# Kernel optimization log

Measured on AMD Instinct MI355X. Metric: run time of the kernel, lower is better.

Reference implementation:

```python
import jax, jax.numpy as jnp
import numpy as np

N_HEADS = 16
NEG_FILL = -1000000000.0  # masked_fill value from the torch module
PADDING = 0.0             # default padding arg


def setup_inputs() -> dict:
    key = jax.random.key(0)
    kq, kk, kv = jax.random.split(key, 3)
    B, S, D = 2, 2048, 1024
    q = jax.random.normal(kq, (B, S, D), dtype=jnp.float32)
    k = jax.random.normal(kk, (B, S, D), dtype=jnp.float32)
    v = jax.random.normal(kv, (B, S, D), dtype=jnp.float32)
    return {"q": q, "k": k, "v": v, "is_masked": 1}


def reference(q, k, v, is_masked):
    B, S, D = q.shape
    d_key = D // N_HEADS

    def split_heads(x):  # [B,S,D] -> [B,H,S,d_key]
        return x.reshape(B, S, N_HEADS, d_key).transpose(0, 2, 1, 3)

    qh, kh, vh = split_heads(q), split_heads(k), split_heads(v)
    scale = 1.0 / jnp.sqrt(jnp.asarray(d_key, dtype=q.dtype))
    # [B,H,S,S] raw attention scores
    scores = jnp.einsum("bhqd,bhkd->bhqk", qh, kh) * scale
    # value-based mask: keep positions where score != padding
    mask = scores != PADDING
    if is_masked:
        causal = jnp.tril(jnp.ones((S, S), dtype=bool))  # [S,S]
        mask = mask & causal
    scores = jnp.where(mask, scores, jnp.asarray(NEG_FILL, dtype=scores.dtype))
    probs = jax.nn.softmax(scores, axis=-1)
    out = jnp.einsum("bhqk,bhkd->bhqd", probs, vh)  # [B,H,S,d_key]
    return out.transpose(0, 2, 1, 3).reshape(B, S, D)
```

## Files before the change

### kernel.cpp

```cpp
#include <hip/hip_runtime.h>
#include <hip/hip_bf16.h>
#include <math.h>

typedef __bf16   bf16x8 __attribute__((ext_vector_type(8)));
typedef _Float16 f16x4  __attribute__((ext_vector_type(4)));
typedef float    f32x4  __attribute__((ext_vector_type(4)));

#define S_LEN 2048
#define D_MODEL 1024
#define LT 72
#define CEXP 0.18033688011112042f

__device__ __forceinline__ float fast_exp2(float x) {
    return __builtin_amdgcn_exp2f(x);
}

template<bool BF>
__device__ __forceinline__ void body(
    const void* __restrict__ qv, const void* __restrict__ kv,
    const void* __restrict__ vv, void* __restrict__ outv,
    int maskflag, int z, int bh,
    __bf16* Ks0, __bf16* Ks1, _Float16* Vt0, _Float16* Vt1)
{
    const int b    = bh >> 4;
    const int h    = bh & 15;
    const int t    = threadIdx.x;
    const int w    = t >> 6;
    const int lane = t & 63;
    const int m16  = lane & 15;
    const int quad = lane >> 4;

    const int q0 = z * 64;
    const size_t head_off = (size_t)b * S_LEN * D_MODEL + (size_t)h * 64;

    const __bf16* qb = (const __bf16*)qv; const float* qf = (const float*)qv;
    const __bf16* kb = (const __bf16*)kv; const float* kf = (const float*)kv;
    const __bf16* vb = (const __bf16*)vv; const float* vf = (const float*)vv;

    bf16x8 aq0, aq1;
    {
        const int r = q0 + w * 16 + m16;
        if (BF) {
            const __bf16* p = qb + head_off + (size_t)r * D_MODEL;
            aq0 = *(const bf16x8*)&p[quad * 8];
            aq1 = *(const bf16x8*)&p[32 + quad * 8];
            #pragma unroll
            for (int j = 0; j < 8; ++j) {
                aq0[j] = (__bf16)((float)aq0[j] * CEXP);
                aq1[j] = (__bf16)((float)aq1[j] * CEXP);
            }
        } else {
            const float* p = qf + head_off + (size_t)r * D_MODEL;
            #pragma unroll
            for (int half = 0; half < 2; ++half) {
                float4 x0 = *(const float4*)&p[half * 32 + quad * 8];
                float4 x1 = *(const float4*)&p[half * 32 + quad * 8 + 4];
                bf16x8 f = { (__bf16)(x0.x*CEXP), (__bf16)(x0.y*CEXP),
                             (__bf16)(x0.z*CEXP), (__bf16)(x0.w*CEXP),
                             (__bf16)(x1.x*CEXP), (__bf16)(x1.y*CEXP),
                             (__bf16)(x1.z*CEXP), (__bf16)(x1.w*CEXP) };
                if (half == 0) aq0 = f; else aq1 = f;
            }
        }
    }

    f32x4 o[4];
    #pragma unroll
    for (int i = 0; i < 4; ++i) o[i] = (f32x4){0.f,0.f,0.f,0.f};
    float lsum = 0.f;

    const int kg = t >> 4, dg = t & 15;
    const int k0 = kg * 4, d0 = dg * 4;
    const int cst = k0 ^ ((dg & 7) << 3);

    const int ktmax = maskflag ? z : (S_LEN / 64 - 1);

    float4 kr[4], vr[4];
    auto pref = [&](int kt) {
        if (BF) {
            const __bf16* base = kb + head_off + (size_t)kt * 64 * D_MODEL;
            #pragma unroll
            for (int i = 0; i < 2; ++i) {
                int c = t + i * 256, row = c >> 3, off = (c & 7) << 3;
                *(uint4*)&kr[i] = *(const uint4*)&base[(size_t)row * D_MODEL + off];
            }
            const __bf16* vp = vb + head_off + (size_t)(kt * 64 + k0) * D_MODEL + d0;
            #pragma unroll
            for (int j = 0; j < 4; ++j)
                *(uint2*)&vr[j] = *(const uint2*)&vp[(size_t)j * D_MODEL];
        } else {
            const float* base = kf + head_off + (size_t)kt * 64 * D_MODEL;
            #pragma unroll
            for (int i = 0; i < 4; ++i) {
                int c = t + i * 256, row = c >> 4, off = (c & 15) << 2;
                kr[i] = *(const float4*)&base[(size_t)row * D_MODEL + off];
            }
            const float* vp = vf + head_off + (size_t)(kt * 64 + k0) * D_MODEL + d0;
            #pragma unroll
            for (int j = 0; j < 4; ++j)
                vr[j] = *(const float4*)&vp[(size_t)j * D_MODEL];
        }
    };
    auto stage = [&](__bf16* Ks, _Float16* Vt) {
        if (BF) {
            #pragma unroll
            for (int i = 0; i < 2; ++i) {
                int c = t + i * 256, row = c >> 3, off = (c & 7) << 3;
                *(uint4*)&Ks[row * LT + off] = *(const uint4*)&kr[i];
            }
            union { uint2 u; __bf16 hh[4]; } r[4];
            #pragma unroll
            for (int j = 0; j < 4; ++j) r[j].u = *(const uint2*)&vr[j];
            #pragma unroll
            for (int j = 0; j < 4; ++j) {
                _Float16 pk[4] = { (_Float16)(float)r[0].hh[j], (_Float16)(float)r[1].hh[j],
                                   (_Float16)(float)r[2].hh[j], (_Float16)(float)r[3].hh[j] };
                *(uint2*)&Vt[(d0 + j) * LT + cst] = *(uint2*)pk;
            }
        } else {
            #pragma unroll
            for (int i = 0; i < 4; ++i) {
                int c = t + i * 256, row = c >> 4, off = (c & 15) << 2;
                float4 ld = kr[i];
                __bf16 pk[4] = { (__bf16)ld.x, (__bf16)ld.y, (__bf16)ld.z, (__bf16)ld.w };
                *(uint2*)&Ks[row * LT + off] = *(uint2*)pk;
            }
            #pragma unroll
            for (int j = 0; j < 4; ++j) {
                _Float16 pk[4] = { (_Float16)vr[0][j], (_Float16)vr[1][j],
                                   (_Float16)vr[2][j], (_Float16)vr[3][j] };
                *(uint2*)&Vt[(d0 + j) * LT + cst] = *(uint2*)pk;
            }
        }
    };

    pref(0);
    for (int kt = 0; kt <= ktmax; ++kt) {
        __bf16*   Ks = (kt & 1) ? Ks1 : Ks0;
        _Float16* Vt = (kt & 1) ? Vt1 : Vt0;
        stage(Ks, Vt);
        __syncthreads();
        if (kt < ktmax) pref(kt + 1);

        f32x4 s[4];
        #pragma unroll
        for (int nt = 0; nt < 4; ++nt) {
            bf16x8 bk0 = *(bf16x8*)&Ks[(nt * 16 + m16) * LT + quad * 8];
            bf16x8 bk1 = *(bf16x8*)&Ks[(nt * 16 + m16) * LT + 32 + quad * 8];
            f32x4 acc = (f32x4){0.f,0.f,0.f,0.f};
            acc = __builtin_amdgcn_mfma_f32_16x16x32_bf16(bk0, aq0, acc, 0, 0, 0);
            acc = __builtin_amdgcn_mfma_f32_16x16x32_bf16(bk1, aq1, acc, 0, 0, 0);
            s[nt] = acc;
        }

        const bool diag = maskflag && (kt == z);
        const int qloc = w * 16 + m16;
        #pragma unroll
        for (int g = 0; g < 4; ++g) {
            f16x4 apv;
            #pragma unroll
            for (int reg = 0; reg < 4; ++reg) {
                float raw = s[g][reg];
                float p = fast_exp2(raw);
                if (diag) {
                    bool valid = (raw != 0.0f) && ((g * 16 + quad * 4 + reg) <= qloc);
                    p = valid ? p : 0.0f;
                }
                lsum += p;
                apv[reg] = (_Float16)p;
            }
            #pragma unroll
            for (int dt = 0; dt < 4; ++dt) {
                const int dim = dt * 16 + m16;
                const int sw = ((dim >> 2) & 7) << 3;
                f16x4 bv = *(f16x4*)&Vt[dim * LT + ((g * 16 + quad * 4) ^ sw)];
                o[dt] = __builtin_amdgcn_mfma_f32_16x16x16f16(apv, bv, o[dt], 0, 0, 0);
            }
        }
    }

    float l = lsum;
    l += __shfl_xor(l, 16, 64);
    l += __shfl_xor(l, 32, 64);
    #pragma unroll
    for (int reg = 0; reg < 4; ++reg) {
        float li = __shfl(l, quad * 4 + reg, 64);
        float invl = 1.0f / li;
        int srow = q0 + w * 16 + quad * 4 + reg;
        #pragma unroll
        for (int dt = 0; dt < 4; ++dt) {
            size_t idx = head_off + (size_t)srow * D_MODEL + dt * 16 + m16;
            float val = o[dt][reg] * invl;
            if (BF) ((__bf16*)outv)[idx] = (__bf16)val;
            else    ((float*)outv)[idx]  = val;
        }
    }
}

__global__ __launch_bounds__(256, 4)
void mha_flash_kernel(const void* __restrict__ qv,
                      const void* __restrict__ kv,
                      const void* __restrict__ vv,
                      const int* __restrict__ is_masked_p,
                      void* __restrict__ outv)
{
    __shared__ __attribute__((aligned(16))) __bf16   Ks0[64 * LT];
    __shared__ __attribute__((aligned(16))) __bf16   Ks1[64 * LT];
    __shared__ __attribute__((aligned(16))) _Float16 Vt0[64 * LT];
    __shared__ __attribute__((aligned(16))) _Float16 Vt1[64 * LT];

    const int id  = blockIdx.x;
    const int xcd = id & 7;
    const int r   = id >> 3;
    const int bh  = xcd * 4 + (r & 3);
    const int u   = r >> 2;
    const int a   = u >> 3, bb = u & 7;
    const int z   = (a == 0) ? bb : (a == 1) ? (15 - bb)
                   : (a == 2) ? (16 + bb) : (31 - bb);

    const int maskflag = *is_masked_p;

    const __bf16* qprobe = (const __bf16*)qv;
    float px = (float)qprobe[2 * (threadIdx.x & 63)];
    bool okp = (px == px) && (fabsf(px) > 1e-6f) && (fabsf(px) < 100.0f);
    unsigned long long bal = __ballot(okp);
    const bool isbf16 = (__popcll(bal) >= 48);

    if (isbf16)
        body<true >(qv, kv, vv, outv, maskflag, z, bh, Ks0, Ks1, Vt0, Vt1);
    else
        body<false>(qv, kv, vv, outv, maskflag, z, bh, Ks0, Ks1, Vt0, Vt1);
}

extern "C" void kernel_launch(void* const* d_in, const int* in_sizes, int n_in,
                              void* d_out, int out_size, void* d_ws, size_t ws_size,
                              hipStream_t stream) {
    const int* is_masked = (const int*)d_in[3];
    mha_flash_kernel<<<dim3(1024), 256, 0, stream>>>(d_in[0], d_in[1], d_in[2], is_masked, d_out);
}
```

Measured before the change: 131.8 us.

## Pair causal query tiles z and 31-z per block to share K/V staging

Each block now processes two query tiles, z and its causal mirror 31-z, so every block does the same amount of work. The K/V tiles staged in shared memory are reused by both query tiles, which halves K/V global loads and staging per output. The grid shrinks from 1024 to 512 blocks and launch bounds drop to 2 blocks per SM, trading occupancy for more registers (two sets of accumulators and Q fragments). Without the mask the pairing still holds, but nothing is balanced by it.

```diff
diff --git a/kernel.cpp b/kernel.cpp
--- a/kernel.cpp
+++ b/kernel.cpp
@@ -30,50 +30,64 @@
     const int m16  = lane & 15;
     const int quad = lane >> 4;
 
-    const int q0 = z * 64;
+    const int qtA = z, qtB = 31 - z;
+    const int q0A = qtA * 64, q0B = qtB * 64;
+
     const size_t head_off = (size_t)b * S_LEN * D_MODEL + (size_t)h * 64;
 
     const __bf16* qb = (const __bf16*)qv; const float* qf = (const float*)qv;
     const __bf16* kb = (const __bf16*)kv; const float* kf = (const float*)kv;
     const __bf16* vb = (const __bf16*)vv; const float* vf = (const float*)vv;
 
-    bf16x8 aq0, aq1;
+    bf16x8 aqA0, aqA1, aqB0, aqB1;
     {
-        const int r = q0 + w * 16 + m16;
+        const int rA = q0A + w * 16 + m16, rB = q0B + w * 16 + m16;
         if (BF) {
-            const __bf16* p = qb + head_off + (size_t)r * D_MODEL;
-            aq0 = *(const bf16x8*)&p[quad * 8];
-            aq1 = *(const bf16x8*)&p[32 + quad * 8];
+            const __bf16* pA = qb + head_off + (size_t)rA * D_MODEL;
+            const __bf16* pB = qb + head_off + (size_t)rB * D_MODEL;
+            aqA0 = *(const bf16x8*)&pA[quad * 8];
+            aqA1 = *(const bf16x8*)&pA[32 + quad * 8];
+            aqB0 = *(const bf16x8*)&pB[quad * 8];
+            aqB1 = *(const bf16x8*)&pB[32 + quad * 8];
             #pragma unroll
             for (int j = 0; j < 8; ++j) {
-                aq0[j] = (__bf16)((float)aq0[j] * CEXP);
-                aq1[j] = (__bf16)((float)aq1[j] * CEXP);
+                aqA0[j] = (__bf16)((float)aqA0[j] * CEXP);
+                aqA1[j] = (__bf16)((float)aqA1[j] * CEXP);
+                aqB0[j] = (__bf16)((float)aqB0[j] * CEXP);
+                aqB1[j] = (__bf16)((float)aqB1[j] * CEXP);
             }
         } else {
-            const float* p = qf + head_off + (size_t)r * D_MODEL;
+            const float* pA = qf + head_off + (size_t)rA * D_MODEL;
+            const float* pB = qf + head_off + (size_t)rB * D_MODEL;
             #pragma unroll
             for (int half = 0; half < 2; ++half) {
-                float4 x0 = *(const float4*)&p[half * 32 + quad * 8];
-                float4 x1 = *(const float4*)&p[half * 32 + quad * 8 + 4];
-                bf16x8 f = { (__bf16)(x0.x*CEXP), (__bf16)(x0.y*CEXP),
-                             (__bf16)(x0.z*CEXP), (__bf16)(x0.w*CEXP),
-                             (__bf16)(x1.x*CEXP), (__bf16)(x1.y*CEXP),
-                             (__bf16)(x1.z*CEXP), (__bf16)(x1.w*CEXP) };
-                if (half == 0) aq0 = f; else aq1 = f;
+                float4 x0 = *(const float4*)&pA[half * 32 + quad * 8];
+                float4 x1 = *(const float4*)&pA[half * 32 + quad * 8 + 4];
+                float4 y0 = *(const float4*)&pB[half * 32 + quad * 8];
+                float4 y1 = *(const float4*)&pB[half * 32 + quad * 8 + 4];
+                bf16x8 fa = { (__bf16)(x0.x*CEXP), (__bf16)(x0.y*CEXP),
+                              (__bf16)(x0.z*CEXP), (__bf16)(x0.w*CEXP),
+                              (__bf16)(x1.x*CEXP), (__bf16)(x1.y*CEXP),
+                              (__bf16)(x1.z*CEXP), (__bf16)(x1.w*CEXP) };
+                bf16x8 fb = { (__bf16)(y0.x*CEXP), (__bf16)(y0.y*CEXP),
+                              (__bf16)(y0.z*CEXP), (__bf16)(y0.w*CEXP),
+                              (__bf16)(y1.x*CEXP), (__bf16)(y1.y*CEXP),
+                              (__bf16)(y1.z*CEXP), (__bf16)(y1.w*CEXP) };
+                if (half == 0) { aqA0 = fa; aqB0 = fb; } else { aqA1 = fa; aqB1 = fb; }
             }
         }
     }
 
-    f32x4 o[4];
+    f32x4 oA[4], oB[4];
     #pragma unroll
-    for (int i = 0; i < 4; ++i) o[i] = (f32x4){0.f,0.f,0.f,0.f};
-    float lsum = 0.f;
+    for (int i = 0; i < 4; ++i) { oA[i] = (f32x4){0.f,0.f,0.f,0.f}; oB[i] = oA[i]; }
+    float lsumA = 0.f, lsumB = 0.f;
 
     const int kg = t >> 4, dg = t & 15;
     const int k0 = kg * 4, d0 = dg * 4;
     const int cst = k0 ^ ((dg & 7) << 3);
 
-    const int ktmax = maskflag ? z : (S_LEN / 64 - 1);
+    const int ktmax = maskflag ? qtB : (S_LEN / 64 - 1);
 
     float4 kr[4], vr[4];
     auto pref = [&](int kt) {
@@ -133,6 +147,8 @@
             }
         }
     };
+
+    const int qloc = w * 16 + m16;
 
     pref(0);
     for (int kt = 0; kt <= ktmax; ++kt) {
@@ -142,62 +158,96 @@
         __syncthreads();
         if (kt < ktmax) pref(kt + 1);
 
-        f32x4 s[4];
+        const bool activeA = (!maskflag) || (kt <= qtA);
+        const bool diagA = maskflag && (kt == qtA);
+        const bool diagB = maskflag && (kt == qtB);
+
+        f32x4 sA[4], sB[4];
         #pragma unroll
         for (int nt = 0; nt < 4; ++nt) {
             bf16x8 bk0 = *(bf16x8*)&Ks[(nt * 16 + m16) * LT + quad * 8];
             bf16x8 bk1 = *(bf16x8*)&Ks[(nt * 16 + m16) * LT + 32 + quad * 8];
             f32x4 acc = (f32x4){0.f,0.f,0.f,0.f};
-            acc = __builtin_amdgcn_mfma_f32_16x16x32_bf16(bk0, aq0, acc, 0, 0, 0);
-            acc = __builtin_amdgcn_mfma_f32_16x16x32_bf16(bk1, aq1, acc, 0, 0, 0);
-            s[nt] = acc;
-        }
-
-        const bool diag = maskflag && (kt == z);
-        const int qloc = w * 16 + m16;
+            acc = __builtin_amdgcn_mfma_f32_16x16x32_bf16(bk0, aqB0, acc, 0, 0, 0);
+            acc = __builtin_amdgcn_mfma_f32_16x16x32_bf16(bk1, aqB1, acc, 0, 0, 0);
+            sB[nt] = acc;
+            if (activeA) {
+                f32x4 acc2 = (f32x4){0.f,0.f,0.f,0.f};
+                acc2 = __builtin_amdgcn_mfma_f32_16x16x32_bf16(bk0, aqA0, acc2, 0, 0, 0);
+                acc2 = __builtin_amdgcn_mfma_f32_16x16x32_bf16(bk1, aqA1, acc2, 0, 0, 0);
+                sA[nt] = acc2;
+            }
+        }
+
         #pragma unroll
         for (int g = 0; g < 4; ++g) {
-            f16x4 apv;
-            #pragma unroll
-            for (int reg = 0; reg < 4; ++reg) {
-                float raw = s[g][reg];
-                float p = fast_exp2(raw);
-                if (diag) {
-                    bool valid = (raw != 0.0f) && ((g * 16 + quad * 4 + reg) <= qloc);
-                    p = valid ? p : 0.0f;
-                }
-                lsum += p;
-                apv[reg] = (_Float16)p;
-            }
+            f16x4 bv[4];
             #pragma unroll
             for (int dt = 0; dt < 4; ++dt) {
                 const int dim = dt * 16 + m16;
                 const int sw = ((dim >> 2) & 7) << 3;
-                f16x4 bv = *(f16x4*)&Vt[dim * LT + ((g * 16 + quad * 4) ^ sw)];
-                o[dt] = __builtin_amdgcn_mfma_f32_16x16x16f16(apv, bv, o[dt], 0, 0, 0);
+                bv[dt] = *(f16x4*)&Vt[dim * LT + ((g * 16 + quad * 4) ^ sw)];
+            }
+            {
+                f16x4 ap;
+                #pragma unroll
+                for (int reg = 0; reg < 4; ++reg) {
+                    float raw = sB[g][reg];
+                    float p = fast_exp2(raw);
+                    if (diagB) {
+                        bool valid = (raw != 0.0f) && ((g * 16 + quad * 4 + reg) <= qloc);
+                        p = valid ? p : 0.0f;
+                    }
+                    lsumB += p;
+                    ap[reg] = (_Float16)p;
+                }
+                #pragma unroll
+                for (int dt = 0; dt < 4; ++dt)
+                    oB[dt] = __builtin_amdgcn_mfma_f32_16x16x16f16(ap, bv[dt], oB[dt], 0, 0, 0);
+            }
+            if (activeA) {
+                f16x4 ap;
+                #pragma unroll
+                for (int reg = 0; reg < 4; ++reg) {
+                    float raw = sA[g][reg];
+                    float p = fast_exp2(raw);
+                    if (diagA) {
+                        bool valid = (raw != 0.0f) && ((g * 16 + quad * 4 + reg) <= qloc);
+                        p = valid ? p : 0.0f;
+                    }
+                    lsumA += p;
+                    ap[reg] = (_Float16)p;
+                }
+                #pragma unroll
+                for (int dt = 0; dt < 4; ++dt)
+                    oA[dt] = __builtin_amdgcn_mfma_f32_16x16x16f16(ap, bv[dt], oA[dt], 0, 0, 0);
             }
         }
     }
 
-    float l = lsum;
-    l += __shfl_xor(l, 16, 64);
-    l += __shfl_xor(l, 32, 64);
-    #pragma unroll
-    for (int reg = 0; reg < 4; ++reg) {
-        float li = __shfl(l, quad * 4 + reg, 64);
-        float invl = 1.0f / li;
-        int srow = q0 + w * 16 + quad * 4 + reg;
+    auto epilogue = [&](f32x4* o, float lsum, int q0) {
+        float l = lsum;
+        l += __shfl_xor(l, 16, 64);
+        l += __shfl_xor(l, 32, 64);
         #pragma unroll
-        for (int dt = 0; dt < 4; ++dt) {
-            size_t idx = head_off + (size_t)srow * D_MODEL + dt * 16 + m16;
-            float val = o[dt][reg] * invl;
-            if (BF) ((__bf16*)outv)[idx] = (__bf16)val;
-            else    ((float*)outv)[idx]  = val;
-        }
-    }
-}
-
-__global__ __launch_bounds__(256, 4)
+        for (int reg = 0; reg < 4; ++reg) {
+            float li = __shfl(l, quad * 4 + reg, 64);
+            float invl = 1.0f / li;
+            int srow = q0 + w * 16 + quad * 4 + reg;
+            #pragma unroll
+            for (int dt = 0; dt < 4; ++dt) {
+                size_t idx = head_off + (size_t)srow * D_MODEL + dt * 16 + m16;
+                float val = o[dt][reg] * invl;
+                if (BF) ((__bf16*)outv)[idx] = (__bf16)val;
+                else    ((float*)outv)[idx]  = val;
+            }
+        }
+    };
+    epilogue(oB, lsumB, q0B);
+    epilogue(oA, lsumA, q0A);
+}
+
+__global__ __launch_bounds__(256, 2)
 void mha_flash_kernel(const void* __restrict__ qv,
                       const void* __restrict__ kv,
                       const void* __restrict__ vv,
@@ -213,10 +263,7 @@
     const int xcd = id & 7;
     const int r   = id >> 3;
     const int bh  = xcd * 4 + (r & 3);
-    const int u   = r >> 2;
-    const int a   = u >> 3, bb = u & 7;
-    const int z   = (a == 0) ? bb : (a == 1) ? (15 - bb)
-                   : (a == 2) ? (16 + bb) : (31 - bb);
+    const int z   = r >> 2;
 
     const int maskflag = *is_masked_p;
 
@@ -236,5 +283,5 @@
                               void* d_out, int out_size, void* d_ws, size_t ws_size,
                               hipStream_t stream) {
     const int* is_masked = (const int*)d_in[3];
-    mha_flash_kernel<<<dim3(1024), 256, 0, stream>>>(d_in[0], d_in[1], d_in[2], is_masked, d_out);
-}
+    mha_flash_kernel<<<dim3(512), 256, 0, stream>>>(d_in[0], d_in[1], d_in[2], is_masked, d_out);
+}
```

Result: faster. 129.1 us (-2.1%).
